# Kernel optimization log

Measured on AMD Instinct MI355X. Metric: run time of the kernel, lower is better.

## Reference

```python
import jax, jax.numpy as jnp
import numpy as np

N_HEAD = 16
N_KV_HEADS = 4
HEAD_SIZE = 128  # n_embd // n_head = 2048 // 16


def setup_inputs() -> dict:
    key = jax.random.key(0)
    k0, k1, k2 = jax.random.split(key, 3)
    B, T, C = 4, 2048, 2048
    kv_dim = N_KV_HEADS * HEAD_SIZE  # 512
    x = jax.random.normal(k0, (B, T, C), dtype=jnp.float32)
    W_attn = jax.random.normal(k1, (C, C + 2 * kv_dim), dtype=jnp.float32) * 0.02
    b_attn = jnp.zeros((C + 2 * kv_dim,), dtype=jnp.float32)
    W_proj = jax.random.normal(k2, (C, C), dtype=jnp.float32) * 0.02
    b_proj = jnp.zeros((C,), dtype=jnp.float32)
    return {"x": x, "W_attn": W_attn, "b_attn": b_attn, "W_proj": W_proj, "b_proj": b_proj}


def reference(x, W_attn, b_attn, W_proj, b_proj):
    B, T, C = x.shape
    hs = HEAD_SIZE
    kv_dim = N_KV_HEADS * hs
    qkv = x @ W_attn + b_attn                      # [B,T,C+2*kv_dim]
    q, k, v = jnp.split(qkv, [C, C + kv_dim], axis=2)
    q = q.reshape(B, T, N_HEAD, hs).transpose(0, 2, 1, 3)       # [B,H,T,hs]
    k = k.reshape(B, T, N_KV_HEADS, hs).transpose(0, 2, 1, 3)   # [B,Hkv,T,hs]
    v = v.reshape(B, T, N_KV_HEADS, hs).transpose(0, 2, 1, 3)
    # GQA: repeat_interleave kv heads to match query heads
    rep = N_HEAD // N_KV_HEADS
    k_r = jnp.repeat(k, rep, axis=1)               # [B,H,T,hs]
    v_r = jnp.repeat(v, rep, axis=1)
    scale = 1.0 / jnp.sqrt(jnp.float32(hs))
    scores = jnp.einsum('bhqd,bhkd->bhqk', q, k_r) * scale      # [B,H,T,T]
    causal = jnp.tril(jnp.ones((T, T), dtype=bool))
    scores = jnp.where(causal, scores, jnp.finfo(scores.dtype).min)
    attn = jax.nn.softmax(scores, axis=-1)
    y = jnp.einsum('bhqk,bhkd->bhqd', attn, v_r)   # [B,H,T,hs]
    y = y.transpose(0, 2, 1, 3).reshape(B, T, C)
    y = y @ W_proj + b_proj
    return y
```

## Files before the change

### kernel.cpp

```cpp
#include <hip/hip_runtime.h>
#include <stdint.h>

#define DEVI __device__ __forceinline__

typedef __attribute__((ext_vector_type(8))) uint16_t u16x8;
typedef __attribute__((ext_vector_type(4))) uint16_t u16x4v;
typedef __attribute__((ext_vector_type(4))) uint32_t u32x4;
typedef __attribute__((ext_vector_type(8))) __bf16 bf16x8;
typedef __attribute__((ext_vector_type(4))) float f32x4;
typedef __attribute__((ext_vector_type(16))) float f32x16;

DEVI uint16_t f2bf(float x) {
  union { float f; uint32_t u; } v; v.f = x;
  return (uint16_t)((v.u + 0x7fffu + ((v.u >> 16) & 1u)) >> 16);
}

DEVI uint16_t f2bfn(float f) {
  __bf16 h = (__bf16)f;
  return __builtin_bit_cast(uint16_t, h);
}

DEVI f32x4 mfma16(u16x8 a, u16x8 b, f32x4 c) {
  return __builtin_amdgcn_mfma_f32_16x16x32_bf16(
      __builtin_bit_cast(bf16x8, a), __builtin_bit_cast(bf16x8, b), c, 0, 0, 0);
}

DEVI f32x16 mfma32(u16x8 a, u16x8 b, f32x16 c) {
  return __builtin_amdgcn_mfma_f32_32x32x16_bf16(
      __builtin_bit_cast(bf16x8, a), __builtin_bit_cast(bf16x8, b), c, 0, 0, 0);
}

DEVI void async16(void* lds, const void* g) {
  __builtin_amdgcn_global_load_lds(
      (const __attribute__((address_space(1))) uint32_t*)g,
      (__attribute__((address_space(3))) uint32_t*)lds, 16, 0, 0);
}

#define QSC 0.12751742925f

__global__ void cvt_f32_bf16(const float* __restrict__ in, uint16_t* __restrict__ out, int n4) {
  int i = blockIdx.x * blockDim.x + threadIdx.x;
  const int st = gridDim.x * blockDim.x;
  for (; i < n4; i += st) {
    float4 v = ((const float4*)in)[i];
    u16x4v o;
    o[0] = f2bf(v.x); o[1] = f2bf(v.y); o[2] = f2bf(v.z); o[3] = f2bf(v.w);
    ((u16x4v*)out)[i] = o;
  }
}

__global__ void transp_cvt(const float* __restrict__ in, uint16_t* __restrict__ out,
                           int K, int N) {
  __shared__ float Ws[64][65];
  const int n0 = blockIdx.x * 64, k0 = blockIdx.y * 64;
  const int t = threadIdx.x;
  const int r = t >> 4, c = (t & 15) << 2;
#pragma unroll
  for (int it = 0; it < 4; ++it) {
    float4 v = *(const float4*)&in[(size_t)(k0 + it * 16 + r) * N + n0 + c];
    Ws[it * 16 + r][c] = v.x; Ws[it * 16 + r][c + 1] = v.y;
    Ws[it * 16 + r][c + 2] = v.z; Ws[it * 16 + r][c + 3] = v.w;
  }
  __syncthreads();
#pragma unroll
  for (int it = 0; it < 4; ++it) {
    const int rr = it * 16 + r;
    const int cc = c;
    ushort4 o;
    o.x = f2bf(Ws[cc][rr]);     o.y = f2bf(Ws[cc + 1][rr]);
    o.z = f2bf(Ws[cc + 2][rr]); o.w = f2bf(Ws[cc + 3][rr]);
    *(ushort4*)&out[(size_t)(n0 + rr) * K + k0 + cc] = o;
  }
}

__global__ void transp_v(const uint16_t* __restrict__ in, uint16_t* __restrict__ out, int T) {
  __shared__ uint16_t Vsm[64][72];
  const int t0 = blockIdx.x * 64, d0 = blockIdx.y * 64, bh = blockIdx.z;
  const uint16_t* ip = in + (size_t)bh * T * 128;
  uint16_t* op = out + (size_t)bh * 128 * T;
  const int t = threadIdx.x;
  const int r = t >> 3, c = (t & 7) << 3;
#pragma unroll
  for (int it = 0; it < 2; ++it) {
    u16x8 v = *(const u16x8*)&ip[(size_t)(t0 + it * 32 + r) * 128 + d0 + c];
#pragma unroll
    for (int j = 0; j < 8; ++j) Vsm[it * 32 + r][c + j] = v[j];
  }
  __syncthreads();
#pragma unroll
  for (int it = 0; it < 2; ++it) {
    const int rr = it * 32 + r;
    const int cc = c;
    u16x8 o;
#pragma unroll
    for (int j = 0; j < 8; ++j) o[j] = Vsm[cc + j][rr];
    *(u16x8*)&op[(size_t)(d0 + rr) * T + t0 + cc] = o;
  }
}

__global__ __launch_bounds__(512, 1)
void gemm_qkv(const uint16_t* __restrict__ A, const uint16_t* __restrict__ Bt,
              const float* __restrict__ bias,
              uint16_t* __restrict__ q, uint16_t* __restrict__ kk, uint16_t* __restrict__ v,
              int M, int N, int K) {
  constexpr int BK = 64;
  __shared__ uint16_t As[2][256 * BK];
  __shared__ uint16_t Bs[2][128 * BK];
  int bid = (int)blockIdx.x;
  const int q8 = (int)gridDim.x >> 3;
  bid = (bid & 7) * q8 + (bid >> 3);
  const int nbn = N >> 7;
  const int brow = (bid / nbn) << 8;
  const int bcol = (bid % nbn) << 7;
  const int t = threadIdx.x;
  const int wid = t >> 6, lane = t & 63;
  const int wm = wid >> 1, wn = wid & 1;
  const int lr = lane & 15, g = lane >> 4, l7 = lr & 7;

  const int logch = (((t & 7) ^ ((t >> 3) & 7)) << 3);
  const uint16_t* Asrc = A + (size_t)(brow + (t >> 3)) * K + logch;
  const uint16_t* Bsrc = Bt + (size_t)(bcol + (t >> 3)) * K + logch;
  const size_t skip64 = (size_t)64 * K;
  const int dt = t * 8;

  auto stageA = [&](int buf, int k0) {
#pragma unroll
    for (int l = 0; l < 4; ++l)
      async16(&As[buf][l * 4096 + dt], Asrc + (size_t)l * skip64 + k0);
  };
  auto stageB = [&](int buf, int k0) {
#pragma unroll
    for (int l = 0; l < 2; ++l)
      async16(&Bs[buf][l * 4096 + dt], Bsrc + (size_t)l * skip64 + k0);
  };

  f32x4 acc[4][4];
#pragma unroll
  for (int i = 0; i < 4; ++i)
#pragma unroll
    for (int j = 0; j < 4; ++j) acc[i][j] = f32x4{0.f, 0.f, 0.f, 0.f};

  const int nt = K / BK;
  stageA(0, 0); stageB(0, 0);
  if (nt > 1) stageB(1, BK);
  asm volatile("s_waitcnt vmcnt(0)" ::: "memory");
  __builtin_amdgcn_s_barrier();

  for (int tt = 0; tt < nt; ++tt) {
    const int buf = tt & 1;
    u16x8 bfr[4][2];
#pragma unroll
    for (int p = 0; p < 2; ++p) {
      if (p == 0) {
#pragma unroll
        for (int j = 0; j < 4; ++j) {
          const int brw = wn * 64 + j * 16 + lr;
#pragma unroll
          for (int s = 0; s < 2; ++s)
            bfr[j][s] = *(const u16x8*)&Bs[buf][brw * 64 + ((((s << 2) + g) ^ l7) << 3)];
        }
      }
      u16x8 af[2][2];
#pragma unroll
      for (int ii = 0; ii < 2; ++ii) {
        const int arow = wm * 64 + (p * 2 + ii) * 16 + lr;
#pragma unroll
        for (int s = 0; s < 2; ++s)
          af[ii][s] = *(const u16x8*)&As[buf][arow * 64 + ((((s << 2) + g) ^ l7) << 3)];
      }
      if (p == 0) {
        if (tt + 1 < nt) stageA(buf ^ 1, (tt + 1) * BK);
      } else {
        if (tt + 2 < nt) {
          stageB(buf, (tt + 2) * BK);
          asm volatile("s_waitcnt vmcnt(2)" ::: "memory");
        } else {
          asm volatile("s_waitcnt vmcnt(0)" ::: "memory");
        }
      }
      __builtin_amdgcn_s_barrier();
      __builtin_amdgcn_s_setprio(1);
#pragma unroll
      for (int ii = 0; ii < 2; ++ii)
#pragma unroll
        for (int j = 0; j < 4; ++j)
#pragma unroll
          for (int s = 0; s < 2; ++s)
            acc[p * 2 + ii][j] = mfma16(af[ii][s], bfr[j][s], acc[p * 2 + ii][j]);
      __builtin_amdgcn_s_setprio(0);
      __builtin_amdgcn_s_barrier();
    }
  }

#pragma unroll
  for (int i = 0; i < 4; ++i) {
#pragma unroll
    for (int j = 0; j < 4; ++j) {
      const int col = bcol + wn * 64 + j * 16 + lr;
      const float bb = bias[col];
#pragma unroll
      for (int r = 0; r < 4; ++r) {
        const int row = brow + wm * 64 + i * 16 + (g << 2) + r;
        const float val = acc[i][j][r] + bb;
        const int b_ = row >> 11, tt2 = row & 2047;
        const int d = col & 127;
        if (col < 2048) {
          const int hh = col >> 7;
          q[((size_t)((b_ * 16 + hh) * 2048 + tt2) << 7) + d] = f2bf(val * QSC);
        } else if (col < 2560) {
          const int hh = (col - 2048) >> 7;
          kk[((size_t)((b_ * 4 + hh) * 2048 + tt2) << 7) + d] = f2bf(val);
        } else {
          const int hh = (col - 2560) >> 7;
          v[((size_t)((b_ * 4 + hh) * 2048 + tt2) << 7) + d] = f2bf(val);
        }
      }
    }
  }
}

__global__ __launch_bounds__(512, 1)
void gemm_proj(const uint16_t* __restrict__ A, const uint16_t* __restrict__ Bt,
               const float* __restrict__ bias, float* __restrict__ outF,
               int M, int N, int K) {
  constexpr int BK = 64;
  __shared__ uint16_t As[2][256 * BK];
  __shared__ uint16_t Bs[2][256 * BK];
  int bid = (int)blockIdx.x;
  const int q8 = (int)gridDim.x >> 3;
  bid = (bid & 7) * q8 + (bid >> 3);
  const int nbn = N >> 8;
  const int brow = (bid / nbn) << 8;
  const int bcol = (bid % nbn) << 8;
  const int t = threadIdx.x;
  const int wid = t >> 6, lane = t & 63;
  const int wm = wid >> 2, wn = wid & 3;
  const int lr = lane & 15, g = lane >> 4;
  const int l7 = lr & 7;

  const int sr0 = t >> 3;
  const int logch = (((t & 7) ^ ((t >> 3) & 7)) << 3);
  const uint16_t* Asrc0 = A + (size_t)(brow + sr0) * K + logch;
  const uint16_t* Asrc1 = A + (size_t)(brow + 64 + sr0) * K + logch;
  const uint16_t* Bsrc0 = Bt + (size_t)(bcol + sr0) * K + logch;
  const uint16_t* Bsrc1 = Bt + (size_t)(bcol + 64 + sr0) * K + logch;
  const size_t hskip = (size_t)128 * K;
  const int d0 = t * 8, d1 = 4096 + t * 8;

  auto stageA = [&](int buf, int h, int k0) {
    async16(&As[buf][h * 8192 + d0], Asrc0 + (size_t)h * hskip + k0);
    async16(&As[buf][h * 8192 + d1], Asrc1 + (size_t)h * hskip + k0);
  };
  auto stageB = [&](int buf, int h, int k0) {
    async16(&Bs[buf][h * 8192 + d0], Bsrc0 + (size_t)h * hskip + k0);
    async16(&Bs[buf][h * 8192 + d1], Bsrc1 + (size_t)h * hskip + k0);
  };

  f32x4 acc[8][4];
#pragma unroll
  for (int i = 0; i < 8; ++i)
#pragma unroll
    for (int j = 0; j < 4; ++j) acc[i][j] = f32x4{0.f, 0.f, 0.f, 0.f};

  const int nt = K / BK;
  stageA(0, 0, 0); stageA(0, 1, 0);
  stageB(0, 0, 0); stageB(0, 1, 0);
  if (nt > 1) { stageB(1, 0, BK); stageB(1, 1, BK); }
  asm volatile("s_waitcnt vmcnt(0)" ::: "memory");
  __builtin_amdgcn_s_barrier();

  for (int tt = 0; tt < nt; ++tt) {
    const int buf = tt & 1;
    u16x8 bfr[4][2];
#pragma unroll
    for (int p = 0; p < 4; ++p) {
      if (p == 0) {
#pragma unroll
        for (int j = 0; j < 4; ++j) {
          const int brw = wn * 64 + j * 16 + lr;
#pragma unroll
          for (int s = 0; s < 2; ++s)
            bfr[j][s] = *(const u16x8*)&Bs[buf][brw * 64 + ((((s << 2) + g) ^ l7) << 3)];
        }
      }
      u16x8 af[2][2];
#pragma unroll
      for (int ii = 0; ii < 2; ++ii) {
        const int arow = wm * 128 + (p * 2 + ii) * 16 + lr;
#pragma unroll
        for (int s = 0; s < 2; ++s)
          af[ii][s] = *(const u16x8*)&As[buf][arow * 64 + ((((s << 2) + g) ^ l7) << 3)];
      }
      if (p == 0) { if (tt + 1 < nt) stageA(buf ^ 1, 0, (tt + 1) * BK); }
      if (p == 1) { if (tt + 1 < nt) stageA(buf ^ 1, 1, (tt + 1) * BK); }
      if (p == 2) { if (tt + 2 < nt) stageB(buf, 0, (tt + 2) * BK); }
      if (p == 3) {
        if (tt + 2 < nt) {
          stageB(buf, 1, (tt + 2) * BK);
          asm volatile("s_waitcnt vmcnt(4)" ::: "memory");
        } else {
          asm volatile("s_waitcnt vmcnt(0)" ::: "memory");
        }
      }
      __builtin_amdgcn_s_barrier();
      __builtin_amdgcn_s_setprio(1);
#pragma unroll
      for (int ii = 0; ii < 2; ++ii)
#pragma unroll
        for (int j = 0; j < 4; ++j)
#pragma unroll
          for (int s = 0; s < 2; ++s)
            acc[p * 2 + ii][j] = mfma16(af[ii][s], bfr[j][s], acc[p * 2 + ii][j]);
      __builtin_amdgcn_s_setprio(0);
      __builtin_amdgcn_s_barrier();
    }
  }

#pragma unroll
  for (int i = 0; i < 8; ++i) {
#pragma unroll
    for (int j = 0; j < 4; ++j) {
      const int col = bcol + wn * 64 + j * 16 + lr;
      const float bb = bias[col];
#pragma unroll
      for (int r = 0; r < 4; ++r) {
        const int row = brow + wm * 128 + i * 16 + (g << 2) + r;
        outF[(size_t)row * N + col] = acc[i][j][r] + bb;
      }
    }
  }
}

__global__ __launch_bounds__(512, 1)
void attn_fwd(const uint16_t* __restrict__ Q,
              const uint16_t* __restrict__ Kg,
              const uint16_t* __restrict__ Vt,
              uint16_t* __restrict__ Y,
              int T) {
  __shared__ __align__(16) uint16_t Ks[2][64 * 128];
  __shared__ __align__(16) uint16_t Vs[2][128 * 64];
  const int pr = blockIdx.x;
  const int h = blockIdx.y, b = blockIdx.z;
  const int hkv = h >> 2;

  const int t = threadIdx.x, w = t >> 6, lane = t & 63;
  const int ql = lane & 31, b5 = lane >> 5;
  const int swz = (ql & 7) << 3;

  const uint16_t* Qh = Q + (size_t)(b * 16 + h) * T * 128;
  const uint16_t* Kp = Kg + (size_t)(b * 4 + hkv) * T * 128;
  const uint16_t* Vp = Vt + (size_t)(b * 4 + hkv) * 128 * T;

  auto stage = [&](int buf, int kv0) {
#pragma unroll
    for (int it = 0; it < 2; ++it) {
      const int krow = it * 32 + w * 4 + (lane >> 4);
      const int kcol = ((lane & 15) << 3) ^ ((krow & 7) << 3);
      async16(&Ks[buf][(it * 32 + w * 4) * 128 + lane * 8],
              &Kp[(size_t)(kv0 + krow) * 128 + kcol]);
    }
#pragma unroll
    for (int it = 0; it < 2; ++it) {
      const int vrow = it * 64 + w * 8 + (lane >> 3);
      const int vcol = ((lane & 7) << 3) ^ ((vrow & 7) << 3);
      async16(&Vs[buf][(it * 64 + w * 8) * 64 + lane * 8],
              &Vp[(size_t)vrow * T + kv0 + vcol]);
    }
  };

  for (int half = 0; half < 2; ++half) {
    const int qb = half == 0 ? 7 - pr : pr;
    const uint16_t* Qp = Qh + (size_t)(qb * 256) * 128;
    const int row0 = qb * 256 + w * 32;
    const int qrow = row0 + ql;

    u16x8 qf[8];
#pragma unroll
    for (int kc = 0; kc < 8; ++kc)
      qf[kc] = *(const u16x8*)&Qp[(size_t)(w * 32 + ql) * 128 + kc * 16 + b5 * 8];

    f32x16 o[4];
#pragma unroll
    for (int db = 0; db < 4; ++db)
#pragma unroll
      for (int r = 0; r < 16; ++r) o[db][r] = 0.f;
    float mrow = -3e38f, lrow = 0.f;

    const int ntiles = 4 * qb + 4;
    const int myn = 4 * qb + (w >> 1) + 1;

    stage(0, 0);
    __syncthreads();

    int cur = 0;
    for (int tile = 0; tile < ntiles; ++tile) {
      if (tile + 1 < ntiles) stage(cur ^ 1, (tile + 1) << 6);

      if (tile < myn) {
        const int kv0 = tile << 6;
        f32x16 s[2];
#pragma unroll
        for (int m = 0; m < 2; ++m)
#pragma unroll
          for (int r = 0; r < 16; ++r) s[m][r] = 0.f;
        __builtin_amdgcn_s_setprio(1);
#pragma unroll
        for (int kc = 0; kc < 8; ++kc) {
          const int cc = (kc * 16 + b5 * 8) ^ swz;
          u16x8 k0f = *(const u16x8*)&Ks[cur][ql * 128 + cc];
          u16x8 k1f = *(const u16x8*)&Ks[cur][(32 + ql) * 128 + cc];
          s[0] = mfma32(k0f, qf[kc], s[0]);
          s[1] = mfma32(k1f, qf[kc], s[1]);
        }
        __builtin_amdgcn_s_setprio(0);

        if (kv0 + 63 > row0) {
#pragma unroll
          for (int m = 0; m < 2; ++m)
#pragma unroll
            for (int r = 0; r < 16; ++r) {
              const int kg = kv0 + 32 * m + (r & 3) + 8 * (r >> 2) + 4 * b5;
              if (kg > qrow) s[m][r] = -3e38f;
            }
        }
        float mx = s[0][0];
#pragma unroll
        for (int m = 0; m < 2; ++m)
#pragma unroll
          for (int r = 0; r < 16; ++r) mx = fmaxf(mx, s[m][r]);
        mx = fmaxf(mx, __shfl_xor(mx, 32));
        const float mnew = fmaxf(mrow, mx);
        const float sc = exp2f(mrow - mnew);
        float ps = 0.f;
#pragma unroll
        for (int m = 0; m < 2; ++m)
#pragma unroll
          for (int r = 0; r < 16; ++r) {
            s[m][r] = exp2f(s[m][r] - mnew);
            ps += s[m][r];
          }
        ps += __shfl_xor(ps, 32);
        mrow = mnew;
        lrow = lrow * sc + ps;
        if (!__all(sc == 1.f)) {
#pragma unroll
          for (int db = 0; db < 4; ++db)
#pragma unroll
            for (int r = 0; r < 16; ++r) o[db][r] *= sc;
        }

        u16x8 pa[4];
#pragma unroll
        for (int m = 0; m < 2; ++m) {
          uint32_t pw[4][2];
#pragma unroll
          for (int a = 0; a < 4; ++a)
#pragma unroll
            for (int hh = 0; hh < 2; ++hh)
              pw[a][hh] = (uint32_t)f2bfn(s[m][4 * a + 2 * hh]) |
                          ((uint32_t)f2bfn(s[m][4 * a + 2 * hh + 1]) << 16);
#pragma unroll
          for (int c = 0; c < 2; ++c) {
            uint32_t wd[4];
#pragma unroll
            for (int hh = 0; hh < 2; ++hh) {
              const uint32_t mine  = b5 ? pw[2 * c + 1][hh] : pw[2 * c][hh];
              const uint32_t yours = b5 ? pw[2 * c][hh] : pw[2 * c + 1][hh];
              const uint32_t x = (uint32_t)__shfl_xor((int)yours, 32);
              wd[hh] = b5 ? x : mine;
              wd[2 + hh] = b5 ? mine : x;
            }
            u32x4 tmp = {wd[0], wd[1], wd[2], wd[3]};
            pa[2 * m + c] = __builtin_bit_cast(u16x8, tmp);
          }
        }

        __builtin_amdgcn_s_setprio(1);
#pragma unroll
        for (int db = 0; db < 4; ++db) {
#pragma unroll
          for (int kf = 0; kf < 4; ++kf) {
            u16x8 vf = *(const u16x8*)&Vs[cur][(32 * db + ql) * 64 +
                                              ((kf * 16 + b5 * 8) ^ swz)];
            o[db] = mfma32(vf, pa[kf], o[db]);
          }
        }
        __builtin_amdgcn_s_setprio(0);
      }
      __syncthreads();
      cur ^= 1;
    }

    uint16_t* Yp = Y + ((size_t)(b * T + row0 + ql)) * 2048 + h * 128 + b5 * 4;
    const float inv = 1.f / lrow;
#pragma unroll
    for (int db = 0; db < 4; ++db)
#pragma unroll
      for (int a = 0; a < 4; ++a) {
        u16x4v pk;
#pragma unroll
        for (int r = 0; r < 4; ++r) pk[r] = f2bfn(o[db][4 * a + r] * inv);
        *(u16x4v*)&Yp[db * 32 + a * 8] = pk;
      }
  }
}

extern "C" void kernel_launch(void* const* d_in, const int* in_sizes, int n_in,
                              void* d_out, int out_size, void* d_ws, size_t ws_size,
                              hipStream_t stream) {
  const float* x      = (const float*)d_in[0];
  const float* W_attn = (const float*)d_in[1];
  const float* b_attn = (const float*)d_in[2];
  const float* W_proj = (const float*)d_in[3];
  const float* b_proj = (const float*)d_in[4];
  float* out = (float*)d_out;

  const int B = 4, T = 2048, C = 2048, H = 16, HKV = 4, HS = 128;
  const int M = B * T;
  const int Nqkv = C + 2 * HKV * HS;

  uint8_t* ws = (uint8_t*)d_ws;
  size_t off = 0;
  auto alloc = [&](size_t bytes) {
    void* p = ws + off;
    off += (bytes + 255) & ~(size_t)255;
    return p;
  };
  uint16_t* xb  = (uint16_t*)alloc((size_t)M * C * 2);
  uint16_t* WaT = (uint16_t*)alloc((size_t)Nqkv * C * 2);
  uint16_t* WpT = (uint16_t*)alloc((size_t)C * C * 2);
  uint16_t* qb  = (uint16_t*)alloc((size_t)B * H * T * HS * 2);
  uint16_t* kb  = (uint16_t*)alloc((size_t)B * HKV * T * HS * 2);
  uint16_t* vb  = (uint16_t*)alloc((size_t)B * HKV * T * HS * 2);
  uint16_t* vtb = (uint16_t*)alloc((size_t)B * HKV * HS * T * 2);
  uint16_t* yb  = xb;

  cvt_f32_bf16<<<2048, 256, 0, stream>>>(x, xb, M * C / 4);
  transp_cvt<<<dim3(Nqkv / 64, C / 64), 256, 0, stream>>>(W_attn, WaT, C, Nqkv);
  transp_cvt<<<dim3(C / 64, C / 64), 256, 0, stream>>>(W_proj, WpT, C, C);
  gemm_qkv<<<dim3((M / 256) * (Nqkv / 128)), 512, 0, stream>>>(
      xb, WaT, b_attn, qb, kb, vb, M, Nqkv, C);
  transp_v<<<dim3(T / 64, 2, B * HKV), 256, 0, stream>>>(vb, vtb, T);
  attn_fwd<<<dim3(4, H, B), 512, 0, stream>>>(qb, kb, vtb, yb, T);
  gemm_proj<<<dim3((M / 256) * (C / 256)), 512, 0, stream>>>(
      yb, WpT, b_proj, out, M, C, C);
}
```

Baseline: 347.4 us.

## Split attention into one q-block per workgroup, single-buffer V, defer rescale

The attention grid now launches one workgroup per 256-row query block (8 per head) instead of pairing a long and a short block in one workgroup. V moves to a single LDS buffer that is loaded during the softmax stage, with an extra barrier before PV, which cuts LDS use so two workgroups may fit per CU. A lazy-rescale rule skips the running-max update and output rescale while the new max stays within 8 of the old one. The costs are an extra __syncthreads per tile, weaker load balance across causal blocks, and a small risk to accuracy from the deferred max.

```diff
diff --git a/kernel.cpp b/kernel.cpp
--- a/kernel.cpp
+++ b/kernel.cpp
@@ -338,8 +338,8 @@
               uint16_t* __restrict__ Y,
               int T) {
   __shared__ __align__(16) uint16_t Ks[2][64 * 128];
-  __shared__ __align__(16) uint16_t Vs[2][128 * 64];
-  const int pr = blockIdx.x;
+  __shared__ __align__(16) uint16_t Vs[128 * 64];
+  const int qb = 7 - (int)blockIdx.x;
   const int h = blockIdx.y, b = blockIdx.z;
   const int hkv = h >> 2;
 
@@ -347,162 +347,166 @@
   const int ql = lane & 31, b5 = lane >> 5;
   const int swz = (ql & 7) << 3;
 
-  const uint16_t* Qh = Q + (size_t)(b * 16 + h) * T * 128;
+  const uint16_t* Qp = Q + ((size_t)(b * 16 + h) * T + qb * 256) * 128;
   const uint16_t* Kp = Kg + (size_t)(b * 4 + hkv) * T * 128;
   const uint16_t* Vp = Vt + (size_t)(b * 4 + hkv) * 128 * T;
 
-  auto stage = [&](int buf, int kv0) {
-#pragma unroll
-    for (int it = 0; it < 2; ++it) {
-      const int krow = it * 32 + w * 4 + (lane >> 4);
-      const int kcol = ((lane & 15) << 3) ^ ((krow & 7) << 3);
-      async16(&Ks[buf][(it * 32 + w * 4) * 128 + lane * 8],
-              &Kp[(size_t)(kv0 + krow) * 128 + kcol]);
-    }
-#pragma unroll
-    for (int it = 0; it < 2; ++it) {
-      const int vrow = it * 64 + w * 8 + (lane >> 3);
-      const int vcol = ((lane & 7) << 3) ^ ((vrow & 7) << 3);
-      async16(&Vs[buf][(it * 64 + w * 8) * 64 + lane * 8],
-              &Vp[(size_t)vrow * T + kv0 + vcol]);
-    }
-  };
-
-  for (int half = 0; half < 2; ++half) {
-    const int qb = half == 0 ? 7 - pr : pr;
-    const uint16_t* Qp = Qh + (size_t)(qb * 256) * 128;
-    const int row0 = qb * 256 + w * 32;
-    const int qrow = row0 + ql;
-
-    u16x8 qf[8];
-#pragma unroll
-    for (int kc = 0; kc < 8; ++kc)
-      qf[kc] = *(const u16x8*)&Qp[(size_t)(w * 32 + ql) * 128 + kc * 16 + b5 * 8];
-
-    f32x16 o[4];
-#pragma unroll
-    for (int db = 0; db < 4; ++db)
-#pragma unroll
-      for (int r = 0; r < 16; ++r) o[db][r] = 0.f;
-    float mrow = -3e38f, lrow = 0.f;
-
-    const int ntiles = 4 * qb + 4;
-    const int myn = 4 * qb + (w >> 1) + 1;
-
-    stage(0, 0);
+  auto stageK = [&](int buf, int kv0) {
+#pragma unroll
+    for (int l = 0; l < 2; ++l) {
+      const int s = l * 512 + t;
+      const int row = s >> 4;
+      const int cl = (s & 15) ^ (row & 7);
+      async16(&Ks[buf][s * 8], &Kp[(size_t)(kv0 + row) * 128 + cl * 8]);
+    }
+  };
+  auto stageV = [&](int kv0) {
+#pragma unroll
+    for (int l = 0; l < 2; ++l) {
+      const int s = l * 512 + t;
+      const int row = s >> 3;
+      const int cl = (s & 7) ^ (row & 7);
+      async16(&Vs[s * 8], &Vp[(size_t)row * T + kv0 + cl * 8]);
+    }
+  };
+
+  const int row0 = qb * 256 + w * 32;
+  const int qrow = row0 + ql;
+
+  u16x8 qf[8];
+#pragma unroll
+  for (int kc = 0; kc < 8; ++kc)
+    qf[kc] = *(const u16x8*)&Qp[(size_t)(w * 32 + ql) * 128 + kc * 16 + b5 * 8];
+
+  f32x16 o[4];
+#pragma unroll
+  for (int db = 0; db < 4; ++db)
+#pragma unroll
+    for (int r = 0; r < 16; ++r) o[db][r] = 0.f;
+  float mrow = -3e38f, lrow = 0.f;
+
+  const int ntiles = 4 * qb + 4;
+  const int myn = 4 * qb + (w >> 1) + 1;
+
+  stageK(0, 0);
+  __syncthreads();
+
+  int cur = 0;
+  for (int tile = 0; tile < ntiles; ++tile) {
+    const int kv0 = tile << 6;
+    stageV(kv0);
+    if (tile + 1 < ntiles) stageK(cur ^ 1, (tile + 1) << 6);
+
+    const bool run = tile < myn;
+    f32x16 s[2];
+    u16x8 pa[4];
+    if (run) {
+#pragma unroll
+      for (int m = 0; m < 2; ++m)
+#pragma unroll
+        for (int r = 0; r < 16; ++r) s[m][r] = 0.f;
+      __builtin_amdgcn_s_setprio(1);
+#pragma unroll
+      for (int kc = 0; kc < 8; ++kc) {
+        const int cc = (kc * 16 + b5 * 8) ^ swz;
+        u16x8 k0f = *(const u16x8*)&Ks[cur][ql * 128 + cc];
+        u16x8 k1f = *(const u16x8*)&Ks[cur][(32 + ql) * 128 + cc];
+        s[0] = mfma32(k0f, qf[kc], s[0]);
+        s[1] = mfma32(k1f, qf[kc], s[1]);
+      }
+      __builtin_amdgcn_s_setprio(0);
+
+      if (kv0 + 63 > row0) {
+#pragma unroll
+        for (int m = 0; m < 2; ++m)
+#pragma unroll
+          for (int r = 0; r < 16; ++r) {
+            const int kg = kv0 + 32 * m + (r & 3) + 8 * (r >> 2) + 4 * b5;
+            if (kg > qrow) s[m][r] = -3e38f;
+          }
+      }
+      float mx = s[0][0];
+#pragma unroll
+      for (int m = 0; m < 2; ++m)
+#pragma unroll
+        for (int r = 0; r < 16; ++r) mx = fmaxf(mx, s[m][r]);
+      mx = fmaxf(mx, __shfl_xor(mx, 32));
+      const bool defer = __all(mx <= mrow + 8.f);
+      const float mnew = defer ? mrow : fmaxf(mrow, mx);
+      const float sc = defer ? 1.f : exp2f(mrow - mnew);
+      float ps = 0.f;
+#pragma unroll
+      for (int m = 0; m < 2; ++m)
+#pragma unroll
+        for (int r = 0; r < 16; ++r) {
+          s[m][r] = exp2f(s[m][r] - mnew);
+          ps += s[m][r];
+        }
+      ps += __shfl_xor(ps, 32);
+      mrow = mnew;
+      lrow = lrow * sc + ps;
+      if (!defer) {
+#pragma unroll
+        for (int db = 0; db < 4; ++db)
+#pragma unroll
+          for (int r = 0; r < 16; ++r) o[db][r] *= sc;
+      }
+
+#pragma unroll
+      for (int m = 0; m < 2; ++m) {
+        uint32_t pw[4][2];
+#pragma unroll
+        for (int a = 0; a < 4; ++a)
+#pragma unroll
+          for (int hh = 0; hh < 2; ++hh)
+            pw[a][hh] = (uint32_t)f2bfn(s[m][4 * a + 2 * hh]) |
+                        ((uint32_t)f2bfn(s[m][4 * a + 2 * hh + 1]) << 16);
+#pragma unroll
+        for (int c = 0; c < 2; ++c) {
+          uint32_t wd[4];
+#pragma unroll
+          for (int hh = 0; hh < 2; ++hh) {
+            const uint32_t mine  = b5 ? pw[2 * c + 1][hh] : pw[2 * c][hh];
+            const uint32_t yours = b5 ? pw[2 * c][hh] : pw[2 * c + 1][hh];
+            const uint32_t x = (uint32_t)__shfl_xor((int)yours, 32);
+            wd[hh] = b5 ? x : mine;
+            wd[2 + hh] = b5 ? mine : x;
+          }
+          u32x4 tmp = {wd[0], wd[1], wd[2], wd[3]};
+          pa[2 * m + c] = __builtin_bit_cast(u16x8, tmp);
+        }
+      }
+    }
     __syncthreads();
 
-    int cur = 0;
-    for (int tile = 0; tile < ntiles; ++tile) {
-      if (tile + 1 < ntiles) stage(cur ^ 1, (tile + 1) << 6);
-
-      if (tile < myn) {
-        const int kv0 = tile << 6;
-        f32x16 s[2];
-#pragma unroll
-        for (int m = 0; m < 2; ++m)
-#pragma unroll
-          for (int r = 0; r < 16; ++r) s[m][r] = 0.f;
-        __builtin_amdgcn_s_setprio(1);
-#pragma unroll
-        for (int kc = 0; kc < 8; ++kc) {
-          const int cc = (kc * 16 + b5 * 8) ^ swz;
-          u16x8 k0f = *(const u16x8*)&Ks[cur][ql * 128 + cc];
-          u16x8 k1f = *(const u16x8*)&Ks[cur][(32 + ql) * 128 + cc];
-          s[0] = mfma32(k0f, qf[kc], s[0]);
-          s[1] = mfma32(k1f, qf[kc], s[1]);
-        }
-        __builtin_amdgcn_s_setprio(0);
-
-        if (kv0 + 63 > row0) {
-#pragma unroll
-          for (int m = 0; m < 2; ++m)
-#pragma unroll
-            for (int r = 0; r < 16; ++r) {
-              const int kg = kv0 + 32 * m + (r & 3) + 8 * (r >> 2) + 4 * b5;
-              if (kg > qrow) s[m][r] = -3e38f;
-            }
-        }
-        float mx = s[0][0];
-#pragma unroll
-        for (int m = 0; m < 2; ++m)
-#pragma unroll
-          for (int r = 0; r < 16; ++r) mx = fmaxf(mx, s[m][r]);
-        mx = fmaxf(mx, __shfl_xor(mx, 32));
-        const float mnew = fmaxf(mrow, mx);
-        const float sc = exp2f(mrow - mnew);
-        float ps = 0.f;
-#pragma unroll
-        for (int m = 0; m < 2; ++m)
-#pragma unroll
-          for (int r = 0; r < 16; ++r) {
-            s[m][r] = exp2f(s[m][r] - mnew);
-            ps += s[m][r];
-          }
-        ps += __shfl_xor(ps, 32);
-        mrow = mnew;
-        lrow = lrow * sc + ps;
-        if (!__all(sc == 1.f)) {
-#pragma unroll
-          for (int db = 0; db < 4; ++db)
-#pragma unroll
-            for (int r = 0; r < 16; ++r) o[db][r] *= sc;
-        }
-
-        u16x8 pa[4];
-#pragma unroll
-        for (int m = 0; m < 2; ++m) {
-          uint32_t pw[4][2];
-#pragma unroll
-          for (int a = 0; a < 4; ++a)
-#pragma unroll
-            for (int hh = 0; hh < 2; ++hh)
-              pw[a][hh] = (uint32_t)f2bfn(s[m][4 * a + 2 * hh]) |
-                          ((uint32_t)f2bfn(s[m][4 * a + 2 * hh + 1]) << 16);
-#pragma unroll
-          for (int c = 0; c < 2; ++c) {
-            uint32_t wd[4];
-#pragma unroll
-            for (int hh = 0; hh < 2; ++hh) {
-              const uint32_t mine  = b5 ? pw[2 * c + 1][hh] : pw[2 * c][hh];
-              const uint32_t yours = b5 ? pw[2 * c][hh] : pw[2 * c + 1][hh];
-              const uint32_t x = (uint32_t)__shfl_xor((int)yours, 32);
-              wd[hh] = b5 ? x : mine;
-              wd[2 + hh] = b5 ? mine : x;
-            }
-            u32x4 tmp = {wd[0], wd[1], wd[2], wd[3]};
-            pa[2 * m + c] = __builtin_bit_cast(u16x8, tmp);
-          }
-        }
-
-        __builtin_amdgcn_s_setprio(1);
-#pragma unroll
-        for (int db = 0; db < 4; ++db) {
-#pragma unroll
-          for (int kf = 0; kf < 4; ++kf) {
-            u16x8 vf = *(const u16x8*)&Vs[cur][(32 * db + ql) * 64 +
-                                              ((kf * 16 + b5 * 8) ^ swz)];
-            o[db] = mfma32(vf, pa[kf], o[db]);
-          }
-        }
-        __builtin_amdgcn_s_setprio(0);
-      }
-      __syncthreads();
-      cur ^= 1;
-    }
-
-    uint16_t* Yp = Y + ((size_t)(b * T + row0 + ql)) * 2048 + h * 128 + b5 * 4;
-    const float inv = 1.f / lrow;
-#pragma unroll
-    for (int db = 0; db < 4; ++db)
-#pragma unroll
-      for (int a = 0; a < 4; ++a) {
-        u16x4v pk;
-#pragma unroll
-        for (int r = 0; r < 4; ++r) pk[r] = f2bfn(o[db][4 * a + r] * inv);
-        *(u16x4v*)&Yp[db * 32 + a * 8] = pk;
-      }
-  }
+    if (run) {
+      __builtin_amdgcn_s_setprio(1);
+#pragma unroll
+      for (int db = 0; db < 4; ++db) {
+#pragma unroll
+        for (int kf = 0; kf < 4; ++kf) {
+          u16x8 vf = *(const u16x8*)&Vs[(32 * db + ql) * 64 +
+                                        ((kf * 16 + b5 * 8) ^ swz)];
+          o[db] = mfma32(vf, pa[kf], o[db]);
+        }
+      }
+      __builtin_amdgcn_s_setprio(0);
+    }
+    __syncthreads();
+    cur ^= 1;
+  }
+
+  uint16_t* Yp = Y + ((size_t)(b * T + row0 + ql)) * 2048 + h * 128 + b5 * 4;
+  const float inv = 1.f / lrow;
+#pragma unroll
+  for (int db = 0; db < 4; ++db)
+#pragma unroll
+    for (int a = 0; a < 4; ++a) {
+      u16x4v pk;
+#pragma unroll
+      for (int r = 0; r < 4; ++r) pk[r] = f2bfn(o[db][4 * a + r] * inv);
+      *(u16x4v*)&Yp[db * 32 + a * 8] = pk;
+    }
 }
 
 extern "C" void kernel_launch(void* const* d_in, const int* in_sizes, int n_in,
@@ -541,7 +545,7 @@
   gemm_qkv<<<dim3((M / 256) * (Nqkv / 128)), 512, 0, stream>>>(
       xb, WaT, b_attn, qb, kb, vb, M, Nqkv, C);
   transp_v<<<dim3(T / 64, 2, B * HKV), 256, 0, stream>>>(vb, vtb, T);
-  attn_fwd<<<dim3(4, H, B), 512, 0, stream>>>(qb, kb, vtb, yb, T);
+  attn_fwd<<<dim3(8, H, B), 512, 0, stream>>>(qb, kb, vtb, yb, T);
   gemm_proj<<<dim3((M / 256) * (C / 256)), 512, 0, stream>>>(
       yb, WpT, b_proj, out, M, C, C);
 }
```

New measurement: 416.5 us. 1.2x slower.
